# Performance work log

Measured on AMD Instinct MI355X. Metric: run time of the kernel, lower is better.

The kernel has to match this reference:

```python
import jax, jax.numpy as jnp
import numpy as np

H = 50   # hidden_size
D = 8    # input_size
B = 2048
T = 512


def setup_inputs() -> dict:
    key = jax.random.key(0)
    ks = jax.random.split(key, 11)
    s = 1.0 / np.sqrt(H)  # PyTorch LSTM/Linear default init bound
    u = lambda k, shape: jax.random.uniform(k, shape, jnp.float32, -s, s)
    return {
        "x": jax.random.normal(ks[0], (B, T, D), jnp.float32),
        # layer 0: input 8 -> hidden 50 (gate order i,f,g,o as in PyTorch)
        "Wih0": u(ks[1], (4 * H, D)),
        "Whh0": u(ks[2], (4 * H, H)),
        "bih0": u(ks[3], (4 * H,)),
        "bhh0": u(ks[4], (4 * H,)),
        # layer 1: hidden 50 -> hidden 50
        "Wih1": u(ks[5], (4 * H, H)),
        "Whh1": u(ks[6], (4 * H, H)),
        "bih1": u(ks[7], (4 * H,)),
        "bhh1": u(ks[8], (4 * H,)),
        # final linear 50 -> 1
        "Wlin": u(ks[9], (1, H)),
        "blin": u(ks[10], (1,)),
    }


def _lstm_layer(x, Wih, Whh, b):
    # x: [B, T, Din] -> outputs h over time: [B, T, H]
    Bb = x.shape[0]
    Hh = Whh.shape[1]
    # precompute input-to-gate projection for all timesteps (one big GEMM)
    x_proj = jnp.einsum("btd,gd->btg", x, Wih) + b  # [B, T, 4H]

    def step(carry, xt):
        h, c = carry
        gates = xt + h @ Whh.T  # [B, 4H]
        i, f, g, o = jnp.split(gates, 4, axis=-1)
        i = jax.nn.sigmoid(i)
        f = jax.nn.sigmoid(f)
        g = jnp.tanh(g)
        o = jax.nn.sigmoid(o)
        c = f * c + i * g
        h = o * jnp.tanh(c)
        return (h, c), h

    init = (jnp.zeros((Bb, Hh), x.dtype), jnp.zeros((Bb, Hh), x.dtype))
    _, hs = jax.lax.scan(step, init, jnp.swapaxes(x_proj, 0, 1))  # [T, B, H]
    return jnp.swapaxes(hs, 0, 1)


def reference(x, Wih0, Whh0, bih0, bhh0, Wih1, Whh1, bih1, bhh1, Wlin, blin):
    h1 = _lstm_layer(x, Wih0, Whh0, bih0 + bhh0)   # [B, T, H]
    h2 = _lstm_layer(h1, Wih1, Whh1, bih1 + bhh1)  # [B, T, H]
    last = h2[:, -1, :]                            # [B, H]
    return last @ Wlin.T + blin                    # [B, 1]
```

## Files before the change

kernel.cpp:

```cpp
#include <hip/hip_runtime.h>
#include <math.h>

#define Hn 50
#define Dn 8
#define Tn 512
#define BB 8
#define NBLK 256
#define KST 136

typedef __attribute__((ext_vector_type(8))) short short8;
typedef __attribute__((ext_vector_type(4))) float f32x4;

__device__ __forceinline__ float fexp2_(float x) {
#if __has_builtin(__builtin_amdgcn_exp2f)
    return __builtin_amdgcn_exp2f(x);
#else
    return exp2f(x);
#endif
}
__device__ __forceinline__ float frcp_(float x) {
#if __has_builtin(__builtin_amdgcn_rcpf)
    return __builtin_amdgcn_rcpf(x);
#else
    return 1.0f / x;
#endif
}
__device__ __forceinline__ float sigmoidf_(float x) {
    return frcp_(1.0f + fexp2_(-1.44269504f * x));
}
__device__ __forceinline__ float tanhf_(float x) {
    return 2.0f * sigmoidf_(2.0f * x) - 1.0f;
}
__device__ __forceinline__ float bf2f(short s) {
    return __uint_as_float(((unsigned)(unsigned short)s) << 16);
}
__device__ __forceinline__ void split_bf(float v, short& hi, short& lo) {
    hi = (short)(__float_as_uint(v) >> 16);
    const float r = v - bf2f(hi);
    lo = (short)(__float_as_uint(r) >> 16);
}
__device__ __forceinline__ float lstm_cell4(const f32x4 g4, float& c) {
    c = sigmoidf_(g4.y) * c + sigmoidf_(g4.x) * tanhf_(g4.z);
    return sigmoidf_(g4.w) * tanhf_(c);
}
__device__ __forceinline__ float shflxor8(float v) {
    return __shfl_xor(v, 8, 64);
}


template<int NL1, int NL0, bool XD>
__device__ __forceinline__ void run_loop(
    const int* l1T, const int* l0T,
    int b0, int lane, int quad, int col,
    short (*bP)[16][KST], float* h1f, const float* x,
    const float* Wih0, const float* Whh0, const float* bih0, const float* bhh0,
    const float* Wih1, const float* Whh1, const float* bih1, const float* bhh1)
{
    constexpr int NS = NL1 + NL0;
    constexpr int NPAIR = (NS + 1) / 2;
    constexpr int NBF = (NL1 > 0) ? 4 : 2;

    short8 W1[NL1 > 0 ? NL1 : 1][4][2];
    short8 W0[NL0 > 0 ? NL0 : 1][2][2];
    f32x4  biasv[NS];
    int    kb[NS];
    int    cellb[NS];

    #pragma unroll
    for (int i = 0; i < NL1; ++i) {
        const int T = l1T[i];
        const int ng = T * 16 + col, cl = ng >> 2, g = ng & 3;
        const bool on = (cl < Hn);
        const int grow = g * Hn + cl;
        #pragma unroll
        for (int s = 0; s < 4; ++s)
            #pragma unroll
            for (int j = 0; j < 8; ++j) {
                const int k = 32 * s + quad * 8 + j;
                float v = 0.f;
                if (on) {
                    if (k < Hn)                      v = Wih1[grow * Hn + k];
                    else if (k >= 64 && k < 64 + Hn) v = Whh1[grow * Hn + (k - 64)];
                }
                short hi, lo; split_bf(v, hi, lo);
                W1[i][s][0][j] = hi; W1[i][s][1][j] = lo;
            }
        const int myc = 4 * T + quad;
        #pragma unroll
        for (int r = 0; r < 4; ++r)
            biasv[i][r] = ((myc < Hn) && (col < 8))
                        ? (bih1[r * Hn + myc] + bhh1[r * Hn + myc]) : 0.f;
        kb[i] = 64 + 4 * T; cellb[i] = 4 * T;
    }
    #pragma unroll
    for (int i = 0; i < NL0; ++i) {
        const int T = l0T[i];
        const int ng = T * 16 + col, cl = ng >> 2, g = ng & 3;
        const bool on = (cl < Hn);
        const int grow = g * Hn + cl;
        #pragma unroll
        for (int s = 0; s < 2; ++s)
            #pragma unroll
            for (int j = 0; j < 8; ++j) {
                const int k = 32 * s + quad * 8 + j;
                float v = 0.f;
                if (on) {
                    if (k < Hn)           v = Whh0[grow * Hn + k];
                    else if (k < Hn + Dn) v = Wih0[grow * Dn + (k - Hn)];
                }
                short hi, lo; split_bf(v, hi, lo);
                W0[i][s][0][j] = hi; W0[i][s][1][j] = lo;
            }
        const int myc = 4 * T + quad;
        #pragma unroll
        for (int r = 0; r < 4; ++r)
            biasv[NL1 + i][r] = ((myc < Hn) && (col < 8))
                              ? (bih0[r * Hn + myc] + bhh0[r * Hn + myc]) : 0.f;
        kb[NL1 + i] = 4 * T; cellb[NL1 + i] = 4 * T;
    }

    const short* base0 = &bP[0][0][0];
    const short* base1 = &bP[1][0][0];
    int rdo[NBF];
    #pragma unroll
    for (int s = 0; s < NBF; ++s) rdo[s] = col * KST + 32 * s + quad * 8;

    int  wofH[NPAIR], wofL[NPAIR], wofS[NPAIR];
    bool actOK[NPAIR], lagged[NPAIR];
    #pragma unroll
    for (int p = 0; p < NPAIR; ++p) {
        const int ia = 2 * p;
        const bool hasB = (ia + 1 < NS);
        const int slot = (hasB && col >= 8) ? ia + 1 : ia;
        const int cell = cellb[slot] + quad;
        const int kc   = kb[slot] + quad;
        lagged[p] = (slot < NL1);
        actOK[p]  = (cell < Hn);
        wofH[p] = (col & 7) * KST + kc;
        wofL[p] = wofH[p] + 8 * KST;
        wofS[p] = col * KST + kc;
    }

    float c[NPAIR];
    #pragma unroll
    for (int p = 0; p < NPAIR; ++p) c[p] = 0.f;

    const float* xp = XD ? (x + (size_t)(b0 + (lane >> 3)) * Tn * Dn + (lane & 7))
                         : (const float*)nullptr;

    for (int t = 0; t < Tn; ++t) {
        float xv = 0.f;
        if (XD) { if (t + 1 < Tn) xv = xp[(size_t)(t + 1) * Dn]; }

        const short* rb = (t & 1) ? base1 : base0;
        short* wb = (short*)((t & 1) ? base0 : base1);

        short8 BF[NBF];
        #pragma unroll
        for (int s = 0; s < NBF; ++s)
            BF[s] = *(const short8*)&rb[rdo[s]];

        f32x4 acc[NS];
        #pragma unroll
        for (int i = 0; i < NS; ++i) acc[i] = biasv[i];
        #pragma unroll
        for (int i = 0; i < NL1; ++i)
            #pragma unroll
            for (int s = 0; s < 4; ++s) {
                acc[i] = __builtin_amdgcn_mfma_f32_16x16x32_bf16(W1[i][s][0], BF[s], acc[i], 0, 0, 0);
                acc[i] = __builtin_amdgcn_mfma_f32_16x16x32_bf16(W1[i][s][1], BF[s], acc[i], 0, 0, 0);
            }
        #pragma unroll
        for (int i = 0; i < NL0; ++i)
            #pragma unroll
            for (int s = 0; s < 2; ++s) {
                acc[NL1 + i] = __builtin_amdgcn_mfma_f32_16x16x32_bf16(W0[i][s][0], BF[s], acc[NL1 + i], 0, 0, 0);
                acc[NL1 + i] = __builtin_amdgcn_mfma_f32_16x16x32_bf16(W0[i][s][1], BF[s], acc[NL1 + i], 0, 0, 0);
            }

        #pragma unroll
        for (int p = 0; p < NPAIR; ++p) {
            const int ia = 2 * p;
            const bool hasB = (ia + 1 < NS);
            f32x4 g;
            #pragma unroll
            for (int r = 0; r < 4; ++r) {
                if (hasB) {
                    const float u = (col < 8) ? acc[ia][r]     : acc[ia + 1][r];
                    const float v = (col < 8) ? acc[ia + 1][r] : acc[ia][r];
                    g[r] = u + shflxor8(v);
                } else {
                    g[r] = acc[ia][r] + shflxor8(acc[ia][r]);
                }
            }
            const bool doAct = actOK[p] && ((t >= 1) || !lagged[p]);
            if (doAct) {
                const float h = lstm_cell4(g, c[p]);
                short hi, lo; split_bf(h, hi, lo);
                if (hasB) { wb[wofH[p]] = hi; wb[wofL[p]] = lo; }
                else      { wb[wofS[p]] = (col < 8) ? hi : lo; }
            }
        }
        if (XD) {
            if (t + 1 < Tn) {
                short hi, lo; split_bf(xv, hi, lo);
                wb[(lane >> 3) * KST + Hn + (lane & 7)]       = hi;
                wb[((lane >> 3) + 8) * KST + Hn + (lane & 7)] = lo;
            }
        }
        __syncthreads();
    }

    if constexpr (NL1 > 0) {
        const short* rb = base0;
        short8 BF[4];
        #pragma unroll
        for (int s = 0; s < 4; ++s)
            BF[s] = *(const short8*)&rb[col * KST + 32 * s + quad * 8];
        f32x4 accE[NL1];
        #pragma unroll
        for (int i = 0; i < NL1; ++i) accE[i] = biasv[i];
        #pragma unroll
        for (int i = 0; i < NL1; ++i)
            #pragma unroll
            for (int s = 0; s < 4; ++s) {
                accE[i] = __builtin_amdgcn_mfma_f32_16x16x32_bf16(W1[i][s][0], BF[s], accE[i], 0, 0, 0);
                accE[i] = __builtin_amdgcn_mfma_f32_16x16x32_bf16(W1[i][s][1], BF[s], accE[i], 0, 0, 0);
            }
        #pragma unroll
        for (int p = 0; p < NPAIR; ++p) {
            const int ia = 2 * p;
            if (ia < NL1) {
                const bool bL1 = (ia + 1 < NL1);
                f32x4 g;
                #pragma unroll
                for (int r = 0; r < 4; ++r) {
                    if (bL1) {
                        const float u = (col < 8) ? accE[ia][r]     : accE[ia + 1][r];
                        const float v = (col < 8) ? accE[ia + 1][r] : accE[ia][r];
                        g[r] = u + shflxor8(v);
                    } else {
                        g[r] = accE[ia][r] + shflxor8(accE[ia][r]);
                    }
                }
                int cell; bool mine;
                if (bL1) { cell = ((col < 8) ? cellb[ia] : cellb[ia + 1]) + quad; mine = true; }
                else     { cell = cellb[ia] + quad;                               mine = (col < 8); }
                if (mine && cell < Hn) {
                    const float h = lstm_cell4(g, c[p]);
                    h1f[cell * 8 + (col & 7)] = h;
                }
            }
        }
    }
}

__global__ __launch_bounds__(1024) void lstm2_kernel(
    const float* __restrict__ x,
    const float* __restrict__ Wih0, const float* __restrict__ Whh0,
    const float* __restrict__ bih0, const float* __restrict__ bhh0,
    const float* __restrict__ Wih1, const float* __restrict__ Whh1,
    const float* __restrict__ bih1, const float* __restrict__ bhh1,
    const float* __restrict__ Wlin, const float* __restrict__ blin,
    float* __restrict__ out)
{
    const int tid  = threadIdx.x;
    const int b0   = blockIdx.x * BB;
    const int w    = __builtin_amdgcn_readfirstlane(tid >> 6);
    const int lane = tid & 63;
    const int quad = lane >> 4;
    const int col  = lane & 15;

    __shared__ __align__(16) short bP[2][16][KST];
    __shared__ float h1f[Hn * 8];

    for (int i = tid; i < 2 * 16 * KST; i += 1024) (&bP[0][0][0])[i] = 0;
    __syncthreads();
    if (tid < 64) {
        const int xb = tid >> 3, xd = tid & 7;
        const float f = x[((size_t)(b0 + xb) * Tn + 0) * Dn + xd];
        short hi, lo; split_bf(f, hi, lo);
        bP[0][xb][Hn + xd]     = hi;
        bP[0][xb + 8][Hn + xd] = lo;
    }
    __syncthreads();

    if (w < 8) {
        const int l1t[1] = {w};
        const int l0t[1] = {w};
        run_loop<1, 1, false>(l1t, l0t, b0, lane, quad, col, bP, h1f, x,
                              Wih0, Whh0, bih0, bhh0, Wih1, Whh1, bih1, bhh1);
    } else if (w < 13) {
        const int l1t[1] = {w};
        run_loop<1, 0, false>(l1t, nullptr, b0, lane, quad, col, bP, h1f, x,
                              Wih0, Whh0, bih0, bhh0, Wih1, Whh1, bih1, bhh1);
    } else if (w == 13) {
        const int l0t[2] = {8, 9};
        run_loop<0, 2, false>(nullptr, l0t, b0, lane, quad, col, bP, h1f, x,
                              Wih0, Whh0, bih0, bhh0, Wih1, Whh1, bih1, bhh1);
    } else if (w == 14) {
        const int l0t[2] = {10, 11};
        run_loop<0, 2, false>(nullptr, l0t, b0, lane, quad, col, bP, h1f, x,
                              Wih0, Whh0, bih0, bhh0, Wih1, Whh1, bih1, bhh1);
    } else {
        const int l0t[1] = {12};
        run_loop<0, 1, true>(nullptr, l0t, b0, lane, quad, col, bP, h1f, x,
                             Wih0, Whh0, bih0, bhh0, Wih1, Whh1, bih1, bhh1);
    }
    __syncthreads();

    if (tid < BB) {
        float o = blin[0];
        #pragma unroll
        for (int k = 0; k < Hn; ++k) o += Wlin[k] * h1f[k * 8 + tid];
        out[b0 + tid] = o;
    }
}

extern "C" void kernel_launch(void* const* d_in, const int* in_sizes, int n_in,
                              void* d_out, int out_size, void* d_ws, size_t ws_size,
                              hipStream_t stream) {
    const float* x    = (const float*)d_in[0];
    const float* Wih0 = (const float*)d_in[1];
    const float* Whh0 = (const float*)d_in[2];
    const float* bih0 = (const float*)d_in[3];
    const float* bhh0 = (const float*)d_in[4];
    const float* Wih1 = (const float*)d_in[5];
    const float* Whh1 = (const float*)d_in[6];
    const float* bih1 = (const float*)d_in[7];
    const float* bhh1 = (const float*)d_in[8];
    const float* Wlin = (const float*)d_in[9];
    const float* blin = (const float*)d_in[10];
    float* out = (float*)d_out;

    lstm2_kernel<<<NBLK, 1024, 0, stream>>>(x, Wih0, Whh0, bih0, bhh0,
                                            Wih1, Whh1, bih1, bhh1,
                                            Wlin, blin, out);
}
```

Before: 427.6 us.

## Fold bias and activation scaling into MFMA weights, swizzle LDS, use DPP xor

The gate bias moves into the weight matrix as an extra K column that multiplies a constant-one entry in the shared h buffer. The per-gate exp2 scale factors (-log2e, or -2log2e for the g gate) are pre-multiplied into the weights. This drops the bias accumulator initialisation and the multiplies inside the activation functions. The shared-memory B operand layout is XOR-swizzled to cut bank conflicts on the short8 reads and the scattered h writes, and the lane-xor-8 shuffle is replaced with a DPP row operation. Pre-scaling the weights before the bf16 hi/lo split could change rounding slightly.

```diff
diff --git a/kernel.cpp b/kernel.cpp
--- a/kernel.cpp
+++ b/kernel.cpp
@@ -25,12 +25,6 @@
     return 1.0f / x;
 #endif
 }
-__device__ __forceinline__ float sigmoidf_(float x) {
-    return frcp_(1.0f + fexp2_(-1.44269504f * x));
-}
-__device__ __forceinline__ float tanhf_(float x) {
-    return 2.0f * sigmoidf_(2.0f * x) - 1.0f;
-}
 __device__ __forceinline__ float bf2f(short s) {
     return __uint_as_float(((unsigned)(unsigned short)s) << 16);
 }
@@ -39,12 +33,25 @@
     const float r = v - bf2f(hi);
     lo = (short)(__float_as_uint(r) >> 16);
 }
-__device__ __forceinline__ float lstm_cell4(const f32x4 g4, float& c) {
-    c = sigmoidf_(g4.y) * c + sigmoidf_(g4.x) * tanhf_(g4.z);
-    return sigmoidf_(g4.w) * tanhf_(c);
-}
-__device__ __forceinline__ float shflxor8(float v) {
+__device__ __forceinline__ float lstm_cell4s(const f32x4 g4, float& c) {
+    const float si = frcp_(1.0f + fexp2_(g4.x));
+    const float sf = frcp_(1.0f + fexp2_(g4.y));
+    const float so = frcp_(1.0f + fexp2_(g4.w));
+    const float tg = 2.0f * frcp_(1.0f + fexp2_(g4.z)) - 1.0f;
+    c = sf * c + si * tg;
+    const float tr = frcp_(1.0f + fexp2_(-2.88539008f * c));
+    return so * (2.0f * tr - 1.0f);
+}
+__device__ __forceinline__ float xor8_(float v) {
+#if __has_builtin(__builtin_amdgcn_update_dpp)
+    return __int_as_float(__builtin_amdgcn_update_dpp(
+        0, __float_as_int(v), 0x128 , 0xF, 0xF, true));
+#else
     return __shfl_xor(v, 8, 64);
+#endif
+}
+__device__ __forceinline__ int swz(int r, int k) {
+    return 8 * (((k >> 3) + r + (r >> 3)) & 15) + (k & 7);
 }
 
 
@@ -62,16 +69,17 @@
 
     short8 W1[NL1 > 0 ? NL1 : 1][4][2];
     short8 W0[NL0 > 0 ? NL0 : 1][2][2];
-    f32x4  biasv[NS];
     int    kb[NS];
     int    cellb[NS];
 
+    const float sc = ((col & 3) == 2) ? -2.88539008f : -1.44269504f;
+
     #pragma unroll
     for (int i = 0; i < NL1; ++i) {
         const int T = l1T[i];
-        const int ng = T * 16 + col, cl = ng >> 2, g = ng & 3;
+        const int ng = T * 16 + col, cl = ng >> 2;
         const bool on = (cl < Hn);
-        const int grow = g * Hn + cl;
+        const int grow = (col & 3) * Hn + cl;
         #pragma unroll
         for (int s = 0; s < 4; ++s)
             #pragma unroll
@@ -81,23 +89,20 @@
                 if (on) {
                     if (k < Hn)                      v = Wih1[grow * Hn + k];
                     else if (k >= 64 && k < 64 + Hn) v = Whh1[grow * Hn + (k - 64)];
-                }
+                    else if (k == 127)               v = bih1[grow] + bhh1[grow];
+                }
+                v *= sc;
                 short hi, lo; split_bf(v, hi, lo);
                 W1[i][s][0][j] = hi; W1[i][s][1][j] = lo;
             }
-        const int myc = 4 * T + quad;
-        #pragma unroll
-        for (int r = 0; r < 4; ++r)
-            biasv[i][r] = ((myc < Hn) && (col < 8))
-                        ? (bih1[r * Hn + myc] + bhh1[r * Hn + myc]) : 0.f;
         kb[i] = 64 + 4 * T; cellb[i] = 4 * T;
     }
     #pragma unroll
     for (int i = 0; i < NL0; ++i) {
         const int T = l0T[i];
-        const int ng = T * 16 + col, cl = ng >> 2, g = ng & 3;
+        const int ng = T * 16 + col, cl = ng >> 2;
         const bool on = (cl < Hn);
-        const int grow = g * Hn + cl;
+        const int grow = (col & 3) * Hn + cl;
         #pragma unroll
         for (int s = 0; s < 2; ++s)
             #pragma unroll
@@ -107,15 +112,12 @@
                 if (on) {
                     if (k < Hn)           v = Whh0[grow * Hn + k];
                     else if (k < Hn + Dn) v = Wih0[grow * Dn + (k - Hn)];
-                }
+                    else if (k == 63)     v = bih0[grow] + bhh0[grow];
+                }
+                v *= sc;
                 short hi, lo; split_bf(v, hi, lo);
                 W0[i][s][0][j] = hi; W0[i][s][1][j] = lo;
             }
-        const int myc = 4 * T + quad;
-        #pragma unroll
-        for (int r = 0; r < 4; ++r)
-            biasv[NL1 + i][r] = ((myc < Hn) && (col < 8))
-                              ? (bih0[r * Hn + myc] + bhh0[r * Hn + myc]) : 0.f;
         kb[NL1 + i] = 4 * T; cellb[NL1 + i] = 4 * T;
     }
 
@@ -123,7 +125,8 @@
     const short* base1 = &bP[1][0][0];
     int rdo[NBF];
     #pragma unroll
-    for (int s = 0; s < NBF; ++s) rdo[s] = col * KST + 32 * s + quad * 8;
+    for (int s = 0; s < NBF; ++s)
+        rdo[s] = col * KST + 8 * (((4 * s + quad) + col + (col >> 3)) & 15);
 
     int  wofH[NPAIR], wofL[NPAIR], wofS[NPAIR];
     bool actOK[NPAIR], lagged[NPAIR];
@@ -136,17 +139,25 @@
         const int kc   = kb[slot] + quad;
         lagged[p] = (slot < NL1);
         actOK[p]  = (cell < Hn);
-        wofH[p] = (col & 7) * KST + kc;
-        wofL[p] = wofH[p] + 8 * KST;
-        wofS[p] = col * KST + kc;
+        const int rH = col & 7, rL = rH + 8;
+        wofH[p] = rH * KST + swz(rH, kc);
+        wofL[p] = rL * KST + swz(rL, kc);
+        wofS[p] = col * KST + swz(col, kc);
     }
 
     float c[NPAIR];
     #pragma unroll
     for (int p = 0; p < NPAIR; ++p) c[p] = 0.f;
+    const f32x4 z4 = {0.f, 0.f, 0.f, 0.f};
 
     const float* xp = XD ? (x + (size_t)(b0 + (lane >> 3)) * Tn * Dn + (lane & 7))
                          : (const float*)nullptr;
+    int xwH = 0, xwL = 0;
+    if (XD) {
+        const int xr = lane >> 3, xd = lane & 7;
+        xwH = xr * KST + swz(xr, Hn + xd);
+        xwL = (xr + 8) * KST + swz(xr + 8, Hn + xd);
+    }
 
     for (int t = 0; t < Tn; ++t) {
         float xv = 0.f;
@@ -162,21 +173,23 @@
 
         f32x4 acc[NS];
         #pragma unroll
-        for (int i = 0; i < NS; ++i) acc[i] = biasv[i];
-        #pragma unroll
-        for (int i = 0; i < NL1; ++i)
-            #pragma unroll
-            for (int s = 0; s < 4; ++s) {
+        for (int i = 0; i < NL1; ++i) {
+            acc[i] = __builtin_amdgcn_mfma_f32_16x16x32_bf16(W1[i][0][0], BF[0], z4, 0, 0, 0);
+            acc[i] = __builtin_amdgcn_mfma_f32_16x16x32_bf16(W1[i][0][1], BF[0], acc[i], 0, 0, 0);
+            #pragma unroll
+            for (int s = 1; s < 4; ++s) {
                 acc[i] = __builtin_amdgcn_mfma_f32_16x16x32_bf16(W1[i][s][0], BF[s], acc[i], 0, 0, 0);
                 acc[i] = __builtin_amdgcn_mfma_f32_16x16x32_bf16(W1[i][s][1], BF[s], acc[i], 0, 0, 0);
             }
-        #pragma unroll
-        for (int i = 0; i < NL0; ++i)
-            #pragma unroll
-            for (int s = 0; s < 2; ++s) {
-                acc[NL1 + i] = __builtin_amdgcn_mfma_f32_16x16x32_bf16(W0[i][s][0], BF[s], acc[NL1 + i], 0, 0, 0);
-                acc[NL1 + i] = __builtin_amdgcn_mfma_f32_16x16x32_bf16(W0[i][s][1], BF[s], acc[NL1 + i], 0, 0, 0);
-            }
+        }
+        #pragma unroll
+        for (int i = 0; i < NL0; ++i) {
+            const int ii = NL1 + i;
+            acc[ii] = __builtin_amdgcn_mfma_f32_16x16x32_bf16(W0[i][0][0], BF[0], z4, 0, 0, 0);
+            acc[ii] = __builtin_amdgcn_mfma_f32_16x16x32_bf16(W0[i][0][1], BF[0], acc[ii], 0, 0, 0);
+            acc[ii] = __builtin_amdgcn_mfma_f32_16x16x32_bf16(W0[i][1][0], BF[1], acc[ii], 0, 0, 0);
+            acc[ii] = __builtin_amdgcn_mfma_f32_16x16x32_bf16(W0[i][1][1], BF[1], acc[ii], 0, 0, 0);
+        }
 
         #pragma unroll
         for (int p = 0; p < NPAIR; ++p) {
@@ -188,14 +201,14 @@
                 if (hasB) {
                     const float u = (col < 8) ? acc[ia][r]     : acc[ia + 1][r];
                     const float v = (col < 8) ? acc[ia + 1][r] : acc[ia][r];
-                    g[r] = u + shflxor8(v);
+                    g[r] = u + xor8_(v);
                 } else {
-                    g[r] = acc[ia][r] + shflxor8(acc[ia][r]);
+                    g[r] = acc[ia][r] + xor8_(acc[ia][r]);
                 }
             }
             const bool doAct = actOK[p] && ((t >= 1) || !lagged[p]);
             if (doAct) {
-                const float h = lstm_cell4(g, c[p]);
+                const float h = lstm_cell4s(g, c[p]);
                 short hi, lo; split_bf(h, hi, lo);
                 if (hasB) { wb[wofH[p]] = hi; wb[wofL[p]] = lo; }
                 else      { wb[wofS[p]] = (col < 8) ? hi : lo; }
@@ -204,8 +217,8 @@
         if (XD) {
             if (t + 1 < Tn) {
                 short hi, lo; split_bf(xv, hi, lo);
-                wb[(lane >> 3) * KST + Hn + (lane & 7)]       = hi;
-                wb[((lane >> 3) + 8) * KST + Hn + (lane & 7)] = lo;
+                wb[xwH] = hi;
+                wb[xwL] = lo;
             }
         }
         __syncthreads();
@@ -216,17 +229,18 @@
         short8 BF[4];
         #pragma unroll
         for (int s = 0; s < 4; ++s)
-            BF[s] = *(const short8*)&rb[col * KST + 32 * s + quad * 8];
+            BF[s] = *(const short8*)&rb[rdo[s]];
         f32x4 accE[NL1];
         #pragma unroll
-        for (int i = 0; i < NL1; ++i) accE[i] = biasv[i];
-        #pragma unroll
-        for (int i = 0; i < NL1; ++i)
-            #pragma unroll
-            for (int s = 0; s < 4; ++s) {
+        for (int i = 0; i < NL1; ++i) {
+            accE[i] = __builtin_amdgcn_mfma_f32_16x16x32_bf16(W1[i][0][0], BF[0], z4, 0, 0, 0);
+            accE[i] = __builtin_amdgcn_mfma_f32_16x16x32_bf16(W1[i][0][1], BF[0], accE[i], 0, 0, 0);
+            #pragma unroll
+            for (int s = 1; s < 4; ++s) {
                 accE[i] = __builtin_amdgcn_mfma_f32_16x16x32_bf16(W1[i][s][0], BF[s], accE[i], 0, 0, 0);
                 accE[i] = __builtin_amdgcn_mfma_f32_16x16x32_bf16(W1[i][s][1], BF[s], accE[i], 0, 0, 0);
             }
+        }
         #pragma unroll
         for (int p = 0; p < NPAIR; ++p) {
             const int ia = 2 * p;
@@ -238,16 +252,16 @@
                     if (bL1) {
                         const float u = (col < 8) ? accE[ia][r]     : accE[ia + 1][r];
                         const float v = (col < 8) ? accE[ia + 1][r] : accE[ia][r];
-                        g[r] = u + shflxor8(v);
+                        g[r] = u + xor8_(v);
                     } else {
-                        g[r] = accE[ia][r] + shflxor8(accE[ia][r]);
+                        g[r] = accE[ia][r] + xor8_(accE[ia][r]);
                     }
                 }
                 int cell; bool mine;
                 if (bL1) { cell = ((col < 8) ? cellb[ia] : cellb[ia + 1]) + quad; mine = true; }
                 else     { cell = cellb[ia] + quad;                               mine = (col < 8); }
                 if (mine && cell < Hn) {
-                    const float h = lstm_cell4(g, c[p]);
+                    const float h = lstm_cell4s(g, c[p]);
                     h1f[cell * 8 + (col & 7)] = h;
                 }
             }
@@ -276,12 +290,17 @@
 
     for (int i = tid; i < 2 * 16 * KST; i += 1024) (&bP[0][0][0])[i] = 0;
     __syncthreads();
-    if (tid < 64) {
-        const int xb = tid >> 3, xd = tid & 7;
+    if (tid < 8) {
+        const short one = (short)0x3F80;
+        bP[0][tid][swz(tid, 63)]  = one;  bP[1][tid][swz(tid, 63)]  = one;
+        bP[0][tid][swz(tid, 127)] = one;  bP[1][tid][swz(tid, 127)] = one;
+    } else if (tid >= 64 && tid < 128) {
+        const int q = tid - 64;
+        const int xb = q >> 3, xd = q & 7;
         const float f = x[((size_t)(b0 + xb) * Tn + 0) * Dn + xd];
         short hi, lo; split_bf(f, hi, lo);
-        bP[0][xb][Hn + xd]     = hi;
-        bP[0][xb + 8][Hn + xd] = lo;
+        bP[0][xb][swz(xb, Hn + xd)]         = hi;
+        bP[0][xb + 8][swz(xb + 8, Hn + xd)] = lo;
     }
     __syncthreads();
 
```

Result: slower. 440.7 us (+3.1%).
